# Kernel tuning notes

Hardware: AMD Instinct MI355X
Metric: run time of the kernel (lower is better)

Reference implementation:

```python
import jax, jax.numpy as jnp
import numpy as np

B, N, D, H, L, FF, CLS = 32, 196, 768, 12, 12, 3072, 1000
HD = D // H
EPS = 1e-5


def setup_inputs() -> dict:
    key = jax.random.key(0)
    ks = jax.random.split(key, 8)
    s = 0.02
    return dict(
        x=jax.random.normal(ks[0], (B, N, D), jnp.float32),
        pos_emb=jax.random.normal(ks[1], (1, N, D), jnp.float32) * 0.2,
        qkv_w=jax.random.normal(ks[2], (L, D, 3 * D), jnp.float32) * s,
        qkv_b=jnp.zeros((L, 3 * D), jnp.float32),
        proj_w=jax.random.normal(ks[3], (L, D, D), jnp.float32) * s,
        proj_b=jnp.zeros((L, D), jnp.float32),
        lin1_w=jax.random.normal(ks[4], (L, D, FF), jnp.float32) * s,
        lin1_b=jnp.zeros((L, FF), jnp.float32),
        lin2_w=jax.random.normal(ks[5], (L, FF, D), jnp.float32) * s,
        lin2_b=jnp.zeros((L, D), jnp.float32),
        pre_ln_w=jnp.ones((L, D), jnp.float32),
        pre_ln_b=jnp.zeros((L, D), jnp.float32),
        norm1_w=jnp.ones((L, D), jnp.float32),
        norm1_b=jnp.zeros((L, D), jnp.float32),
        attn_ln_w=jnp.ones((L, H, N, N), jnp.float32),
        attn_ln_b=jnp.zeros((L, H, N, N), jnp.float32),
        final_ln_w=jnp.ones((D,), jnp.float32),
        final_ln_b=jnp.zeros((D,), jnp.float32),
        pool_w=jax.random.normal(ks[6], (D, 1), jnp.float32) * s,
        pool_b=jnp.zeros((1,), jnp.float32),
        fc_w=jax.random.normal(ks[7], (D, CLS), jnp.float32) * s,
        fc_b=jnp.zeros((CLS,), jnp.float32),
    )


def _ln(x, w, b):
    mu = x.mean(-1, keepdims=True)
    var = ((x - mu) ** 2).mean(-1, keepdims=True)
    return (x - mu) * jax.lax.rsqrt(var + EPS) * w + b


def _forward(x, pos_emb, qkv_w, qkv_b, proj_w, proj_b, lin1_w, lin1_b,
             lin2_w, lin2_b, pre_ln_w, pre_ln_b, norm1_w, norm1_b,
             attn_ln_w, attn_ln_b, final_ln_w, final_ln_b,
             pool_w, pool_b, fc_w, fc_b):
    h = x + pos_emb  # (B,N,D)
    params = dict(qw=qkv_w, qb=qkv_b, pw=proj_w, pb=proj_b,
                  l1w=lin1_w, l1b=lin1_b, l2w=lin2_w, l2b=lin2_b,
                  prew=pre_ln_w, preb=pre_ln_b, n1w=norm1_w, n1b=norm1_b,
                  aw=attn_ln_w, ab=attn_ln_b)

    def step(carry, p):
        src, _ = carry
        y = _ln(src, p['prew'], p['preb'])
        qkv = (y @ p['qw'] + p['qb']).reshape(B, N, 3, H, HD)
        qkv = qkv.transpose(2, 0, 3, 1, 4)  # (3,B,H,N,HD)
        q, k, v = qkv[0], qkv[1], qkv[2]
        # grassmanian_point: project each head vector onto the unit sphere
        q = q / jnp.linalg.norm(q, axis=-1, keepdims=True)
        k = k / jnp.linalg.norm(k, axis=-1, keepdims=True)
        # ||q_i outer k_j||^2 over head_dim == sum_d q_id^2 * k_jd^2
        attn = jnp.einsum('bhid,bhjd->bhij', q * q, k * k)  # (B,H,N,N)
        # LayerNorm over (H,N,N) per batch element
        mu = attn.mean(axis=(1, 2, 3), keepdims=True)
        var = ((attn - mu) ** 2).mean(axis=(1, 2, 3), keepdims=True)
        attn = (attn - mu) * jax.lax.rsqrt(var + EPS) * p['aw'] + p['ab']
        out = jnp.einsum('bhij,bhjd->bhid', attn, v)
        out = out.transpose(0, 2, 1, 3).reshape(B, N, D)
        out = out @ p['pw'] + p['pb']
        src = _ln(src + out, p['n1w'], p['n1b'])
        ff = jax.nn.gelu(src @ p['l1w'] + p['l1b'], approximate=False)
        ff = ff @ p['l2w'] + p['l2b']
        return (src + ff, attn), None

    init = (h, jnp.zeros((B, H, N, N), x.dtype))
    (src, attn), _ = jax.lax.scan(step, init, params)
    xf = _ln(src, final_ln_w, final_ln_b)
    a = jax.nn.softmax(xf @ pool_w + pool_b, axis=1)  # (B,N,1) sequence pooling
    pooled = jnp.einsum('bnk,bnd->bd', a, xf)
    logits = pooled @ fc_w + fc_b
    return logits, attn


def reference(x, pos_emb, qkv_w, qkv_b, proj_w, proj_b, lin1_w, lin1_b,
              lin2_w, lin2_b, pre_ln_w, pre_ln_b, norm1_w, norm1_b,
              attn_ln_w, attn_ln_b, final_ln_w, final_ln_b,
              pool_w, pool_b, fc_w, fc_b):
    return _forward(x, pos_emb, qkv_w, qkv_b, proj_w, proj_b, lin1_w, lin1_b,
                    lin2_w, lin2_b, pre_ln_w, pre_ln_b, norm1_w, norm1_b,
                    attn_ln_w, attn_ln_b, final_ln_w, final_ln_b,
                    pool_w, pool_b, fc_w, fc_b)
```

## Files before the change

kernel.cpp:

```cpp
#include <hip/hip_runtime.h>
#include <hip/hip_bf16.h>

typedef unsigned short u16;
typedef __bf16 bf16x8 __attribute__((ext_vector_type(8)));
typedef _Float16 f16x8 __attribute__((ext_vector_type(8)));
typedef float f32x4 __attribute__((ext_vector_type(4)));
typedef u16 u16x8 __attribute__((ext_vector_type(8)));
typedef u16 u16x4 __attribute__((ext_vector_type(4)));

#define B_ 32
#define N_ 196
#define D_ 768
#define H_ 12
#define L_ 12
#define FF_ 3072
#define CLS_ 1000
#define HD_ 64
#define BH_ 384
#define NTOK_ 6272
#define NP_ 224
#define ATTN_PER_B_ 460992
#define NN_ 38416

__device__ inline u16 f2bf(float f){
    __bf16 h = (__bf16)f;
    return __builtin_bit_cast(u16, h);
}
__device__ inline float bf2f(u16 u){
    __bf16 h = __builtin_bit_cast(__bf16, u);
    return (float)h;
}
__device__ inline void split3(float v, u16& s0, u16& s1, u16& s2){
    s0 = f2bf(v);
    float r = v - bf2f(s0);
    s1 = f2bf(r);
    r = r - bf2f(s1);
    s2 = f2bf(r);
}
__device__ inline u16 f2h(float f){
    _Float16 h = (_Float16)f;
    return __builtin_bit_cast(u16, h);
}
__device__ inline float h2f(u16 u){
    _Float16 h = __builtin_bit_cast(_Float16, u);
    return (float)h;
}
__device__ inline void split2h(float v, u16& h0, u16& h1){
    h0 = f2h(v);
    h1 = f2h(v - h2f(h0));
}


__global__ __launch_bounds__(256)
void addpos_kernel(const float* __restrict__ x, const float* __restrict__ pos,
                   float* __restrict__ src){
    size_t gid = (size_t)blockIdx.x * 256 + threadIdx.x;
    size_t e = gid * 4;
    size_t tok = e / D_;
    size_t d = e % D_;
    size_t pe = (tok % N_) * D_ + d;
    float4 a = *(const float4*)(x + e);
    float4 p = *(const float4*)(pos + pe);
    float4 o = make_float4(a.x + p.x, a.y + p.y, a.z + p.z, a.w + p.w);
    *(float4*)(src + e) = o;
}

__global__ __launch_bounds__(256)
void wtrans_kernel(const float* __restrict__ in, u16* __restrict__ o0,
                   u16* __restrict__ o1, int K, int Nn){
    __shared__ float t[32][33];
    int n0 = blockIdx.x * 32, k0 = blockIdx.y * 32;
    int tx = threadIdx.x & 31, ty = threadIdx.x >> 5;
#pragma unroll
    for (int r = 0; r < 4; ++r)
        t[ty + 8*r][tx] = in[(size_t)(k0 + ty + 8*r) * Nn + n0 + tx];
    __syncthreads();
#pragma unroll
    for (int r = 0; r < 4; ++r){
        float v = t[tx][ty + 8*r];
        size_t oi = (size_t)(n0 + ty + 8*r) * K + k0 + tx;
        u16 a, b;
        split2h(v, a, b);
        o0[oi] = a; o1[oi] = b;
    }
}


__global__ __launch_bounds__(256)
void ln_row(const float* __restrict__ in, const float* __restrict__ w,
            const float* __restrict__ bb, float* __restrict__ outF,
            u16* __restrict__ o0, u16* __restrict__ o1){
    int row = blockIdx.x, tid = threadIdx.x;
    const float* base = in + (size_t)row * D_;
    float x0 = base[tid], x1 = base[tid + 256], x2 = base[tid + 512];
    float s = x0 + x1 + x2;
    float q = x0*x0 + x1*x1 + x2*x2;
    __shared__ float red[8];
    for (int o = 32; o > 0; o >>= 1){ s += __shfl_down(s, o); q += __shfl_down(q, o); }
    if ((tid & 63) == 0){ red[tid >> 6] = s; red[4 + (tid >> 6)] = q; }
    __syncthreads();
    s = red[0] + red[1] + red[2] + red[3];
    q = red[4] + red[5] + red[6] + red[7];
    float mu = s * (1.f / D_);
    float rv = rsqrtf(q * (1.f / D_) - mu * mu + 1e-5f);
#pragma unroll
    for (int t = 0; t < 3; ++t){
        int c = tid + t * 256;
        float x = (t == 0 ? x0 : (t == 1 ? x1 : x2));
        float val = (x - mu) * rv * w[c] + bb[c];
        size_t oi = (size_t)row * D_ + c;
        if (outF) outF[oi] = val;
        if (o0){
            u16 a, b;
            split2h(val, a, b);
            o0[oi] = a; o1[oi] = b;
        }
    }
}


template<int EPI>
__global__ __launch_bounds__(256)
void gemm_f16s2(const u16* __restrict__ A0, const u16* __restrict__ A1,
                const u16* __restrict__ B0, const u16* __restrict__ B1,
                const float* __restrict__ bias, const float* __restrict__ res,
                float* __restrict__ outF, u16* __restrict__ oH,
                u16* __restrict__ oL, int M, int Nn, int K){
    __shared__ u16 Lds[2][4][128 * 32];
    const int tid = threadIdx.x;
    const int w = tid >> 6, l = tid & 63;
    const int wr = w >> 1, wc = w & 1;
    const int nwg = gridDim.x;
    const int nbx = Nn >> 7;
    const int orig = blockIdx.x;
    const int qq = nwg >> 3, rr = nwg & 7;
    const int xcd = orig & 7, local = orig >> 3;
    const int wg = (xcd < rr ? xcd * (qq + 1) : rr * (qq + 1) + (xcd - rr) * qq) + local;
    const int m0 = (wg / nbx) * 128, n0 = (wg % nbx) * 128;
    const u16* gsrc = (w == 0 ? A0 : w == 1 ? A1 : w == 2 ? B0 : B1);
    const int rowbase = (w < 2 ? m0 : n0);
    const int lq = (l & 3) ^ ((l >> 3) & 3);
    const u16* gp = gsrc + (size_t)(rowbase + (l >> 2)) * K + lq * 8;
    const size_t gstep = (size_t)16 * K;
    f32x4 acc[4][4] = {};
    const int arow = l & 15;
    const int qsel = l >> 4;
    const int nsteps = K >> 5;

    auto stage = [&](int buf, int k0){
        u16* lbuf = &Lds[buf][w][0];
        const u16* gpk = gp + k0;
#pragma unroll
        for (int i = 0; i < 8; ++i){
            __builtin_amdgcn_global_load_lds(
                (const __attribute__((address_space(1))) unsigned int*)gpk,
                (__attribute__((address_space(3))) unsigned int*)(lbuf + i * 512),
                16, 0, 0);
            gpk += gstep;
        }
    };

    stage(0, 0);
    for (int step = 0; step < nsteps; ++step){
        const int cur = step & 1;
        __syncthreads();
        if (step + 1 < nsteps) stage(1 - cur, (step + 1) << 5);
        f16x8 a0[4], a1[4], b0[4], b1[4];
#pragma unroll
        for (int m = 0; m < 4; ++m){
            int row = wr * 64 + m * 16 + arow;
            int off = row * 32 + ((qsel ^ ((row >> 1) & 3)) * 8);
            a0[m] = __builtin_bit_cast(f16x8, *(const u16x8*)&Lds[cur][0][off]);
            a1[m] = __builtin_bit_cast(f16x8, *(const u16x8*)&Lds[cur][1][off]);
        }
#pragma unroll
        for (int n = 0; n < 4; ++n){
            int row = wc * 64 + n * 16 + arow;
            int off = row * 32 + ((qsel ^ ((row >> 1) & 3)) * 8);
            b0[n] = __builtin_bit_cast(f16x8, *(const u16x8*)&Lds[cur][2][off]);
            b1[n] = __builtin_bit_cast(f16x8, *(const u16x8*)&Lds[cur][3][off]);
        }
#pragma unroll
        for (int m = 0; m < 4; ++m)
#pragma unroll
            for (int n = 0; n < 4; ++n){
                acc[m][n] = __builtin_amdgcn_mfma_f32_16x16x32_f16(a1[m], b0[n], acc[m][n], 0, 0, 0);
                acc[m][n] = __builtin_amdgcn_mfma_f32_16x16x32_f16(a0[m], b1[n], acc[m][n], 0, 0, 0);
                acc[m][n] = __builtin_amdgcn_mfma_f32_16x16x32_f16(a0[m], b0[n], acc[m][n], 0, 0, 0);
            }
    }
    const int r4 = (l >> 4) * 4, c16 = l & 15;
#pragma unroll
    for (int m = 0; m < 4; ++m){
#pragma unroll
        for (int n = 0; n < 4; ++n){
            int colg = n0 + wc*64 + n*16 + c16;
            float bv = bias[colg];
#pragma unroll
            for (int r = 0; r < 4; ++r){
                int rowg = m0 + wr*64 + m*16 + r4 + r;
                size_t oi = (size_t)rowg * Nn + colg;
                float v = acc[m][n][r] + bv;
                if (EPI == 0){
                    outF[oi] = v;
                } else if (EPI == 1){
                    v = 0.5f * v * (1.0f + erff(v * 0.70710678118654752f));
                    u16 a, b;
                    split2h(v, a, b);
                    oH[oi] = a; oL[oi] = b;
                } else {
                    outF[oi] = v + res[oi];
                }
            }
        }
    }
}


__global__ __launch_bounds__(256)
void qkprep_kernel(const float* __restrict__ QKV,
                   u16* __restrict__ Q0, u16* __restrict__ Q1, u16* __restrict__ Q2,
                   u16* __restrict__ K0, u16* __restrict__ K1, u16* __restrict__ K2,
                   u16* __restrict__ VT0, u16* __restrict__ VT1){
    __shared__ float vbuf[NP_][65];
    int bh = blockIdx.x;
    int b = bh / H_, h = bh % H_;
    int w = threadIdx.x >> 6, l = threadIdx.x & 63;
    size_t base = (size_t)bh * (NP_ * HD_);
    for (int n = w; n < NP_; n += 4){
        size_t oi = base + (size_t)n * HD_ + l;
        if (n < N_){
            const float* row = QKV + (size_t)(b * N_ + n) * (3 * D_) + h * HD_;
            float qv = row[l], kv = row[D_ + l], vv = row[2 * D_ + l];
            double qs = (double)qv * (double)qv, ks = (double)kv * (double)kv;
            double qr = qs, kr = ks;
            for (int o = 32; o > 0; o >>= 1){ qr += __shfl_xor(qr, o); kr += __shfl_xor(kr, o); }
            float q2 = (float)(qs / qr), k2 = (float)(ks / kr);
            u16 a, bb, c;
            split3(q2, a, bb, c);
            Q0[oi] = a; Q1[oi] = bb; Q2[oi] = c;
            split3(k2, a, bb, c);
            K0[oi] = a; K1[oi] = bb; K2[oi] = c;
            vbuf[n][l] = vv;
        } else {
            Q0[oi] = 0; Q1[oi] = 0; Q2[oi] = 0;
            K0[oi] = 0; K1[oi] = 0; K2[oi] = 0;
            vbuf[n][l] = 0.f;
        }
    }
    __syncthreads();
    size_t vtb = (size_t)bh * (HD_ * NP_);
    for (int idx = threadIdx.x; idx < HD_ * NP_; idx += 256){
        int d = idx / NP_, n = idx % NP_;
        u16 a, bb;
        split2h(vbuf[n][d], a, bb);
        VT0[vtb + idx] = a; VT1[vtb + idx] = bb;
    }
}


#define SPAD 72

__global__ __launch_bounds__(256)
void score_mfma3(const u16* __restrict__ Q0, const u16* __restrict__ Q1,
                 const u16* __restrict__ Q2,
                 const u16* __restrict__ K0, const u16* __restrict__ K1,
                 const u16* __restrict__ K2,
                 float* __restrict__ S, double2* __restrict__ part){
    __shared__ u16 Ql[3][32][SPAD];
    __shared__ u16 Kl[3][32][SPAD];
    __shared__ double red2[8];
    int i0 = blockIdx.x * 32;
    int bh = blockIdx.y;
    int tid = threadIdx.x;
    size_t base = (size_t)bh * (NP_ * HD_);
    {
        int r = tid >> 3, q = tid & 7;
        size_t src = base + (size_t)(i0 + r) * HD_ + q * 8;
        *(u16x8*)&Ql[0][r][q * 8] = *(const u16x8*)(Q0 + src);
        *(u16x8*)&Ql[1][r][q * 8] = *(const u16x8*)(Q1 + src);
        *(u16x8*)&Ql[2][r][q * 8] = *(const u16x8*)(Q2 + src);
    }
    const int w = tid >> 6, l = tid & 63;
    const int wm = w >> 1, wn = w & 1;
    const int arow = l & 15, kg0 = (l >> 4) * 8;
    const int r4 = (l >> 4) * 4, c16 = l & 15;
    double dsum = 0.0, dsq = 0.0;
    for (int jt = 0; jt < 7; ++jt){
        __syncthreads();
        {
            int r = tid >> 3, q = tid & 7;
            size_t src = base + (size_t)(jt * 32 + r) * HD_ + q * 8;
            *(u16x8*)&Kl[0][r][q * 8] = *(const u16x8*)(K0 + src);
            *(u16x8*)&Kl[1][r][q * 8] = *(const u16x8*)(K1 + src);
            *(u16x8*)&Kl[2][r][q * 8] = *(const u16x8*)(K2 + src);
        }
        __syncthreads();
        f32x4 acc = {};
#pragma unroll
        for (int kk = 0; kk < 2; ++kk){
            int kg = kk * 32 + kg0;
            bf16x8 a0 = __builtin_bit_cast(bf16x8, *(const u16x8*)&Ql[0][wm*16 + arow][kg]);
            bf16x8 a1 = __builtin_bit_cast(bf16x8, *(const u16x8*)&Ql[1][wm*16 + arow][kg]);
            bf16x8 a2 = __builtin_bit_cast(bf16x8, *(const u16x8*)&Ql[2][wm*16 + arow][kg]);
            bf16x8 b0 = __builtin_bit_cast(bf16x8, *(const u16x8*)&Kl[0][wn*16 + arow][kg]);
            bf16x8 b1 = __builtin_bit_cast(bf16x8, *(const u16x8*)&Kl[1][wn*16 + arow][kg]);
            bf16x8 b2 = __builtin_bit_cast(bf16x8, *(const u16x8*)&Kl[2][wn*16 + arow][kg]);
            acc = __builtin_amdgcn_mfma_f32_16x16x32_bf16(a2, b0, acc, 0, 0, 0);
            acc = __builtin_amdgcn_mfma_f32_16x16x32_bf16(a1, b1, acc, 0, 0, 0);
            acc = __builtin_amdgcn_mfma_f32_16x16x32_bf16(a0, b2, acc, 0, 0, 0);
            acc = __builtin_amdgcn_mfma_f32_16x16x32_bf16(a1, b0, acc, 0, 0, 0);
            acc = __builtin_amdgcn_mfma_f32_16x16x32_bf16(a0, b1, acc, 0, 0, 0);
            acc = __builtin_amdgcn_mfma_f32_16x16x32_bf16(a0, b0, acc, 0, 0, 0);
        }
#pragma unroll
        for (int r = 0; r < 4; ++r){
            int i = i0 + wm * 16 + r4 + r;
            int j = jt * 32 + wn * 16 + c16;
            if (i < N_ && j < N_){
                float v = acc[r];
                S[((size_t)bh * N_ + i) * N_ + j] = v;
                dsum += (double)v;
                dsq += (double)v * (double)v;
            }
        }
    }
    for (int o = 32; o > 0; o >>= 1){
        dsum += __shfl_down(dsum, o);
        dsq  += __shfl_down(dsq, o);
    }
    __syncthreads();
    if ((tid & 63) == 0){ red2[tid >> 6] = dsum; red2[4 + (tid >> 6)] = dsq; }
    __syncthreads();
    if (tid == 0){
        int b = bh / H_, h = bh % H_;
        part[(size_t)b * 84 + h * 7 + blockIdx.x] =
            make_double2(red2[0] + red2[1] + red2[2] + red2[3],
                         red2[4] + red2[5] + red2[6] + red2[7]);
    }
}

__global__ __launch_bounds__(64)
void reduceMS_kernel(const double2* __restrict__ part, float2* __restrict__ musig){
    int b = blockIdx.x, tid = threadIdx.x;
    double s = 0.0, q = 0.0;
    for (int i = tid; i < 84; i += 64){
        double2 p = part[(size_t)b * 84 + i];
        s += p.x; q += p.y;
    }
    for (int o = 32; o > 0; o >>= 1){ s += __shfl_down(s, o); q += __shfl_down(q, o); }
    if (tid == 0){
        double mu = s / (double)ATTN_PER_B_;
        double var = q / (double)ATTN_PER_B_ - mu * mu;
        musig[b] = make_float2((float)mu, (float)(1.0 / sqrt(var + 1e-5)));
    }
}


__global__ __launch_bounds__(256)
void attnnorm_f16(float* __restrict__ S, const float* __restrict__ wv,
                  const float* __restrict__ bv, const float2* __restrict__ musig,
                  u16* __restrict__ AS0, u16* __restrict__ AS1, int writeS){
    int gid = blockIdx.x * 256 + threadIdx.x;
    int jg = gid % 56;
    int rem = gid / 56;
    int i = rem % NP_;
    int bh = rem / NP_;
    int b = bh / H_, h = bh % H_;
    float2 ms = musig[b];
    u16x4 p0, p1;
#pragma unroll
    for (int t = 0; t < 4; ++t){
        int j = jg * 4 + t;
        float val = 0.f;
        if (i < N_ && j < N_){
            size_t si = ((size_t)bh * N_ + i) * N_ + j;
            size_t wi = ((size_t)h * N_ + i) * N_ + j;
            float s = S[si];
            val = (s - ms.x) * ms.y * wv[wi] + bv[wi];
            if (writeS) S[si] = val;
        }
        u16 a, bb;
        split2h(val, a, bb);
        p0[t] = a; p1[t] = bb;
    }
    size_t oo = (size_t)bh * (NP_ * NP_) + (size_t)i * NP_ + jg * 4;
    *(u16x4*)&AS0[oo] = p0;
    *(u16x4*)&AS1[oo] = p1;
}


__global__ __launch_bounds__(256)
void pv_f16s2(const u16* __restrict__ AS0, const u16* __restrict__ AS1,
              const u16* __restrict__ VT0, const u16* __restrict__ VT1,
              u16* __restrict__ PA0, u16* __restrict__ PA1){
    __shared__ u16 Al[2][32][40];
    __shared__ u16 Vl[2][64][40];
    int i0 = blockIdx.x * 32;
    int bh = blockIdx.y;
    int b = bh / H_, h = bh % H_;
    int tid = threadIdx.x;
    size_t abase = (size_t)bh * (NP_ * NP_) + (size_t)i0 * NP_;
    size_t vbase = (size_t)bh * (HD_ * NP_);
    const int w = tid >> 6, l = tid & 63;
    const int arow = l & 15, kg0 = (l >> 4) * 8;
    const int r4 = (l >> 4) * 4, c16 = l & 15;
    f32x4 acc[2] = {};
    for (int k0 = 0; k0 < NP_; k0 += 32){
        __syncthreads();
        {
            int s = tid >> 7, rem = tid & 127;
            int r = rem >> 2, q = rem & 3;
            const u16* src = (s == 0 ? AS0 : AS1);
            *(u16x8*)&Al[s][r][q * 8] = *(const u16x8*)(src + abase + (size_t)r * NP_ + k0 + q * 8);
        }
#pragma unroll
        for (int it = 0; it < 2; ++it){
            int c = tid + it * 256;
            int s = c >> 8, rem = c & 255;
            int r = rem >> 2, q = rem & 3;
            const u16* src = (s == 0 ? VT0 : VT1);
            *(u16x8*)&Vl[s][r][q * 8] = *(const u16x8*)(src + vbase + (size_t)r * NP_ + k0 + q * 8);
        }
        __syncthreads();
        f16x8 a0[2], a1[2];
#pragma unroll
        for (int m = 0; m < 2; ++m){
            a0[m] = __builtin_bit_cast(f16x8, *(const u16x8*)&Al[0][m*16 + arow][kg0]);
            a1[m] = __builtin_bit_cast(f16x8, *(const u16x8*)&Al[1][m*16 + arow][kg0]);
        }
        f16x8 b0 = __builtin_bit_cast(f16x8, *(const u16x8*)&Vl[0][w*16 + arow][kg0]);
        f16x8 b1 = __builtin_bit_cast(f16x8, *(const u16x8*)&Vl[1][w*16 + arow][kg0]);
#pragma unroll
        for (int m = 0; m < 2; ++m){
            acc[m] = __builtin_amdgcn_mfma_f32_16x16x32_f16(a1[m], b1, acc[m], 0, 0, 0);
            acc[m] = __builtin_amdgcn_mfma_f32_16x16x32_f16(a1[m], b0, acc[m], 0, 0, 0);
            acc[m] = __builtin_amdgcn_mfma_f32_16x16x32_f16(a0[m], b1, acc[m], 0, 0, 0);
            acc[m] = __builtin_amdgcn_mfma_f32_16x16x32_f16(a0[m], b0, acc[m], 0, 0, 0);
        }
    }
#pragma unroll
    for (int m = 0; m < 2; ++m)
#pragma unroll
        for (int r = 0; r < 4; ++r){
            int i = i0 + m * 16 + r4 + r;
            if (i < N_){
                size_t oi = ((size_t)b * N_ + i) * D_ + h * HD_ + w * 16 + c16;
                u16 s0, s1;
                split2h(acc[m][r], s0, s1);
                PA0[oi] = s0; PA1[oi] = s1;
            }
        }
}


__global__ __launch_bounds__(256)
void rowdot_kernel(const float* __restrict__ xf, const float* __restrict__ pw,
                   const float* __restrict__ pb, float* __restrict__ sraw){
    int row = blockIdx.x, tid = threadIdx.x;
    const float* base = xf + (size_t)row * D_;
    float s = base[tid] * pw[tid] + base[tid + 256] * pw[tid + 256] + base[tid + 512] * pw[tid + 512];
    __shared__ float red[4];
    for (int o = 32; o > 0; o >>= 1) s += __shfl_xor(s, o);
    if ((tid & 63) == 0) red[tid >> 6] = s;
    __syncthreads();
    if (tid == 0) sraw[row] = red[0] + red[1] + red[2] + red[3] + pb[0];
}

__global__ __launch_bounds__(256)
void softmax196_kernel(const float* __restrict__ sraw, float* __restrict__ aw){
    int b = blockIdx.x, tid = threadIdx.x;
    __shared__ float red[8];
    float v = (tid < N_) ? sraw[b * N_ + tid] : -3.0e38f;
    float m = v;
    for (int o = 32; o > 0; o >>= 1) m = fmaxf(m, __shfl_xor(m, o));
    if ((tid & 63) == 0) red[tid >> 6] = m;
    __syncthreads();
    float M = fmaxf(fmaxf(red[0], red[1]), fmaxf(red[2], red[3]));
    float e = (tid < N_) ? expf(v - M) : 0.f;
    float s = e;
    for (int o = 32; o > 0; o >>= 1) s += __shfl_xor(s, o);
    if ((tid & 63) == 0) red[4 + (tid >> 6)] = s;
    __syncthreads();
    float S = red[4] + red[5] + red[6] + red[7];
    if (tid < N_) aw[b * N_ + tid] = e / S;
}

__global__ __launch_bounds__(256)
void poolmat_kernel(const float* __restrict__ aw, const float* __restrict__ xf,
                    float* __restrict__ pooled){
    int b = blockIdx.y;
    int d = blockIdx.x * 256 + threadIdx.x;
    float acc = 0.f;
    for (int n = 0; n < N_; ++n)
        acc += aw[b * N_ + n] * xf[((size_t)b * N_ + n) * D_ + d];
    pooled[b * D_ + d] = acc;
}

__global__ __launch_bounds__(256)
void fc_kernel(const float* __restrict__ pooled, const float* __restrict__ fw,
               const float* __restrict__ fb, float* __restrict__ out){
    int b = blockIdx.y;
    int c = blockIdx.x * 256 + threadIdx.x;
    if (c >= CLS_) return;
    float acc = fb[c];
    for (int d = 0; d < D_; ++d)
        acc += pooled[b * D_ + d] * fw[(size_t)d * CLS_ + c];
    out[b * CLS_ + c] = acc;
}

__global__ __launch_bounds__(256)
void zero_logits(float* __restrict__ out){
    out[blockIdx.x * 256 + threadIdx.x] = 0.f;
}


extern "C" void kernel_launch(void* const* d_in, const int* in_sizes, int n_in,
                              void* d_out, int out_size, void* d_ws, size_t ws_size,
                              hipStream_t stream){
    const float* x        = (const float*)d_in[0];
    const float* pos_emb  = (const float*)d_in[1];
    const float* qkv_w    = (const float*)d_in[2];
    const float* qkv_b    = (const float*)d_in[3];
    const float* proj_w   = (const float*)d_in[4];
    const float* proj_b   = (const float*)d_in[5];
    const float* lin1_w   = (const float*)d_in[6];
    const float* lin1_b   = (const float*)d_in[7];
    const float* lin2_w   = (const float*)d_in[8];
    const float* lin2_b   = (const float*)d_in[9];
    const float* pre_ln_w = (const float*)d_in[10];
    const float* pre_ln_b = (const float*)d_in[11];
    const float* norm1_w  = (const float*)d_in[12];
    const float* norm1_b  = (const float*)d_in[13];
    const float* attn_ln_w= (const float*)d_in[14];
    const float* attn_ln_b= (const float*)d_in[15];
    const float* fln_w    = (const float*)d_in[16];
    const float* fln_b    = (const float*)d_in[17];
    const float* pool_w   = (const float*)d_in[18];
    const float* pool_b   = (const float*)d_in[19];
    const float* fc_w     = (const float*)d_in[20];
    const float* fc_b     = (const float*)d_in[21];

    float* dout = (float*)d_out;
    float* S = dout + (size_t)B_ * CLS_;

    char* ws = (char*)d_ws;
    size_t off = 0;
    auto alloc = [&](size_t bytes)->char*{
        char* p = ws + off;
        off += (bytes + 255) & ~(size_t)255;
        return p;
    };
    float* SRC   = (float*)alloc((size_t)NTOK_ * D_ * 4);
    float* Yb    = (float*)alloc((size_t)NTOK_ * D_ * 4);
    float* TMP   = (float*)alloc((size_t)NTOK_ * D_ * 4);
    float* QKV   = (float*)alloc((size_t)NTOK_ * 3 * D_ * 4);
    u16*   A0    = (u16*)  alloc((size_t)NTOK_ * D_ * 2);
    u16*   A1    = (u16*)  alloc((size_t)NTOK_ * D_ * 2);
    u16*   W0    = (u16*)  alloc((size_t)FF_ * D_ * 2);
    u16*   W1    = (u16*)  alloc((size_t)FF_ * D_ * 2);
    u16*   F0    = (u16*)  alloc((size_t)NTOK_ * FF_ * 2);
    u16*   F1    = (u16*)  alloc((size_t)NTOK_ * FF_ * 2);
    u16*   Q0b   = (u16*)  alloc((size_t)BH_ * NP_ * HD_ * 2);
    u16*   Q1b   = (u16*)  alloc((size_t)BH_ * NP_ * HD_ * 2);
    u16*   Q2b   = (u16*)  alloc((size_t)BH_ * NP_ * HD_ * 2);
    u16*   K0b   = (u16*)  alloc((size_t)BH_ * NP_ * HD_ * 2);
    u16*   K1b   = (u16*)  alloc((size_t)BH_ * NP_ * HD_ * 2);
    u16*   K2b   = (u16*)  alloc((size_t)BH_ * NP_ * HD_ * 2);
    u16*   VT0   = (u16*)  alloc((size_t)BH_ * HD_ * NP_ * 2);
    u16*   VT1   = (u16*)  alloc((size_t)BH_ * HD_ * NP_ * 2);
    double2* PART= (double2*)alloc((size_t)B_ * 84 * 16);
    float2* MUSIG= (float2*)alloc((size_t)B_ * 8);
    float* SRAW  = (float*)alloc((size_t)NTOK_ * 4);
    float* AW    = (float*)alloc((size_t)NTOK_ * 4);
    float* POOLED= (float*)alloc((size_t)B_ * D_ * 4);
    u16* AS0 = F0, *AS1 = F1;

    if (ws_size < off){
        zero_logits<<<(B_ * CLS_) / 256, 256, 0, stream>>>(dout);
        return;
    }

    const int cvt_blocks = NTOK_ * D_ / (256 * 4);
    const int an_blocks = (int)((size_t)BH_ * NP_ * NP_ / (256 * 4));

    addpos_kernel<<<cvt_blocks, 256, 0, stream>>>(x, pos_emb, SRC);

    for (int l = 0; l < L_; ++l){
        const float* qw  = qkv_w  + (size_t)l * D_ * 3 * D_;
        const float* qb  = qkv_b  + (size_t)l * 3 * D_;
        const float* pw  = proj_w + (size_t)l * D_ * D_;
        const float* pb  = proj_b + (size_t)l * D_;
        const float* l1w = lin1_w + (size_t)l * D_ * FF_;
        const float* l1b = lin1_b + (size_t)l * FF_;
        const float* l2w = lin2_w + (size_t)l * FF_ * D_;
        const float* l2b = lin2_b + (size_t)l * D_;
        const float* prw = pre_ln_w + (size_t)l * D_;
        const float* prb = pre_ln_b + (size_t)l * D_;
        const float* n1w = norm1_w + (size_t)l * D_;
        const float* n1b = norm1_b + (size_t)l * D_;
        const float* awl = attn_ln_w + (size_t)l * H_ * N_ * N_;
        const float* abl = attn_ln_b + (size_t)l * H_ * N_ * N_;

        ln_row<<<NTOK_, 256, 0, stream>>>(SRC, prw, prb, nullptr, A0, A1);
        wtrans_kernel<<<dim3(3 * D_ / 32, D_ / 32), 256, 0, stream>>>(qw, W0, W1, D_, 3 * D_);
        gemm_f16s2<0><<<(3 * D_ / 128) * (NTOK_ / 128), 256, 0, stream>>>(
            A0, A1, W0, W1, qb, nullptr, QKV, nullptr, nullptr, NTOK_, 3 * D_, D_);
        qkprep_kernel<<<BH_, 256, 0, stream>>>(QKV, Q0b, Q1b, Q2b, K0b, K1b, K2b,
                                               VT0, VT1);
        score_mfma3<<<dim3(7, BH_), 256, 0, stream>>>(Q0b, Q1b, Q2b, K0b, K1b, K2b,
                                                      S, PART);
        reduceMS_kernel<<<B_, 64, 0, stream>>>(PART, MUSIG);
        attnnorm_f16<<<an_blocks, 256, 0, stream>>>(S, awl, abl, MUSIG, AS0, AS1,
                                                    l == L_ - 1 ? 1 : 0);
        pv_f16s2<<<dim3(7, BH_), 256, 0, stream>>>(AS0, AS1, VT0, VT1, A0, A1);
        wtrans_kernel<<<dim3(D_ / 32, D_ / 32), 256, 0, stream>>>(pw, W0, W1, D_, D_);
        gemm_f16s2<2><<<(D_ / 128) * (NTOK_ / 128), 256, 0, stream>>>(
            A0, A1, W0, W1, pb, SRC, TMP, nullptr, nullptr, NTOK_, D_, D_);
        ln_row<<<NTOK_, 256, 0, stream>>>(TMP, n1w, n1b, SRC, A0, A1);
        wtrans_kernel<<<dim3(FF_ / 32, D_ / 32), 256, 0, stream>>>(l1w, W0, W1, D_, FF_);
        gemm_f16s2<1><<<(FF_ / 128) * (NTOK_ / 128), 256, 0, stream>>>(
            A0, A1, W0, W1, l1b, nullptr, nullptr, F0, F1, NTOK_, FF_, D_);
        wtrans_kernel<<<dim3(D_ / 32, FF_ / 32), 256, 0, stream>>>(l2w, W0, W1, FF_, D_);
        gemm_f16s2<2><<<(D_ / 128) * (NTOK_ / 128), 256, 0, stream>>>(
            F0, F1, W0, W1, l2b, SRC, SRC, nullptr, nullptr, NTOK_, D_, FF_);
    }

    ln_row<<<NTOK_, 256, 0, stream>>>(SRC, fln_w, fln_b, Yb, nullptr, nullptr);
    rowdot_kernel<<<NTOK_, 256, 0, stream>>>(Yb, pool_w, pool_b, SRAW);
    softmax196_kernel<<<B_, 256, 0, stream>>>(SRAW, AW);
    poolmat_kernel<<<dim3(D_ / 256, B_), 256, 0, stream>>>(AW, Yb, POOLED);
    fc_kernel<<<dim3((CLS_ + 255) / 256, B_), 256, 0, stream>>>(POOLED, fc_w, fc_b, dout);
}
```

Measured before the change: 7.306 ms.

## Fuse attention normalization into PV kernel and use f16x2 split for scores

```diff
diff --git a/kernel.cpp b/kernel.cpp
--- a/kernel.cpp
+++ b/kernel.cpp
@@ -2,7 +2,6 @@
 #include <hip/hip_bf16.h>
 
 typedef unsigned short u16;
-typedef __bf16 bf16x8 __attribute__((ext_vector_type(8)));
 typedef _Float16 f16x8 __attribute__((ext_vector_type(8)));
 typedef float f32x4 __attribute__((ext_vector_type(4)));
 typedef u16 u16x8 __attribute__((ext_vector_type(8)));
@@ -22,21 +21,6 @@
 #define ATTN_PER_B_ 460992
 #define NN_ 38416
 
-__device__ inline u16 f2bf(float f){
-    __bf16 h = (__bf16)f;
-    return __builtin_bit_cast(u16, h);
-}
-__device__ inline float bf2f(u16 u){
-    __bf16 h = __builtin_bit_cast(__bf16, u);
-    return (float)h;
-}
-__device__ inline void split3(float v, u16& s0, u16& s1, u16& s2){
-    s0 = f2bf(v);
-    float r = v - bf2f(s0);
-    s1 = f2bf(r);
-    r = r - bf2f(s1);
-    s2 = f2bf(r);
-}
 __device__ inline u16 f2h(float f){
     _Float16 h = (_Float16)f;
     return __builtin_bit_cast(u16, h);
@@ -219,8 +203,8 @@
 
 __global__ __launch_bounds__(256)
 void qkprep_kernel(const float* __restrict__ QKV,
-                   u16* __restrict__ Q0, u16* __restrict__ Q1, u16* __restrict__ Q2,
-                   u16* __restrict__ K0, u16* __restrict__ K1, u16* __restrict__ K2,
+                   u16* __restrict__ Q0, u16* __restrict__ Q1,
+                   u16* __restrict__ K0, u16* __restrict__ K1,
                    u16* __restrict__ VT0, u16* __restrict__ VT1){
     __shared__ float vbuf[NP_][65];
     int bh = blockIdx.x;
@@ -236,15 +220,15 @@
             double qr = qs, kr = ks;
             for (int o = 32; o > 0; o >>= 1){ qr += __shfl_xor(qr, o); kr += __shfl_xor(kr, o); }
             float q2 = (float)(qs / qr), k2 = (float)(ks / kr);
-            u16 a, bb, c;
-            split3(q2, a, bb, c);
-            Q0[oi] = a; Q1[oi] = bb; Q2[oi] = c;
-            split3(k2, a, bb, c);
-            K0[oi] = a; K1[oi] = bb; K2[oi] = c;
+            u16 a, bb;
+            split2h(q2, a, bb);
+            Q0[oi] = a; Q1[oi] = bb;
+            split2h(k2, a, bb);
+            K0[oi] = a; K1[oi] = bb;
             vbuf[n][l] = vv;
         } else {
-            Q0[oi] = 0; Q1[oi] = 0; Q2[oi] = 0;
-            K0[oi] = 0; K1[oi] = 0; K2[oi] = 0;
+            Q0[oi] = 0; Q1[oi] = 0;
+            K0[oi] = 0; K1[oi] = 0;
             vbuf[n][l] = 0.f;
         }
     }
@@ -262,13 +246,11 @@
 #define SPAD 72
 
 __global__ __launch_bounds__(256)
-void score_mfma3(const u16* __restrict__ Q0, const u16* __restrict__ Q1,
-                 const u16* __restrict__ Q2,
+void score_f16s2(const u16* __restrict__ Q0, const u16* __restrict__ Q1,
                  const u16* __restrict__ K0, const u16* __restrict__ K1,
-                 const u16* __restrict__ K2,
                  float* __restrict__ S, double2* __restrict__ part){
-    __shared__ u16 Ql[3][32][SPAD];
-    __shared__ u16 Kl[3][32][SPAD];
+    __shared__ u16 Ql[2][32][SPAD];
+    __shared__ u16 Kl[2][32][SPAD];
     __shared__ double red2[8];
     int i0 = blockIdx.x * 32;
     int bh = blockIdx.y;
@@ -279,7 +261,6 @@
         size_t src = base + (size_t)(i0 + r) * HD_ + q * 8;
         *(u16x8*)&Ql[0][r][q * 8] = *(const u16x8*)(Q0 + src);
         *(u16x8*)&Ql[1][r][q * 8] = *(const u16x8*)(Q1 + src);
-        *(u16x8*)&Ql[2][r][q * 8] = *(const u16x8*)(Q2 + src);
     }
     const int w = tid >> 6, l = tid & 63;
     const int wm = w >> 1, wn = w & 1;
@@ -293,25 +274,20 @@
             size_t src = base + (size_t)(jt * 32 + r) * HD_ + q * 8;
             *(u16x8*)&Kl[0][r][q * 8] = *(const u16x8*)(K0 + src);
             *(u16x8*)&Kl[1][r][q * 8] = *(const u16x8*)(K1 + src);
-            *(u16x8*)&Kl[2][r][q * 8] = *(const u16x8*)(K2 + src);
         }
         __syncthreads();
         f32x4 acc = {};
 #pragma unroll
         for (int kk = 0; kk < 2; ++kk){
             int kg = kk * 32 + kg0;
-            bf16x8 a0 = __builtin_bit_cast(bf16x8, *(const u16x8*)&Ql[0][wm*16 + arow][kg]);
-            bf16x8 a1 = __builtin_bit_cast(bf16x8, *(const u16x8*)&Ql[1][wm*16 + arow][kg]);
-            bf16x8 a2 = __builtin_bit_cast(bf16x8, *(const u16x8*)&Ql[2][wm*16 + arow][kg]);
-            bf16x8 b0 = __builtin_bit_cast(bf16x8, *(const u16x8*)&Kl[0][wn*16 + arow][kg]);
-            bf16x8 b1 = __builtin_bit_cast(bf16x8, *(const u16x8*)&Kl[1][wn*16 + arow][kg]);
-            bf16x8 b2 = __builtin_bit_cast(bf16x8, *(const u16x8*)&Kl[2][wn*16 + arow][kg]);
-            acc = __builtin_amdgcn_mfma_f32_16x16x32_bf16(a2, b0, acc, 0, 0, 0);
-            acc = __builtin_amdgcn_mfma_f32_16x16x32_bf16(a1, b1, acc, 0, 0, 0);
-            acc = __builtin_amdgcn_mfma_f32_16x16x32_bf16(a0, b2, acc, 0, 0, 0);
-            acc = __builtin_amdgcn_mfma_f32_16x16x32_bf16(a1, b0, acc, 0, 0, 0);
-            acc = __builtin_amdgcn_mfma_f32_16x16x32_bf16(a0, b1, acc, 0, 0, 0);
-            acc = __builtin_amdgcn_mfma_f32_16x16x32_bf16(a0, b0, acc, 0, 0, 0);
+            f16x8 a0 = __builtin_bit_cast(f16x8, *(const u16x8*)&Ql[0][wm*16 + arow][kg]);
+            f16x8 a1 = __builtin_bit_cast(f16x8, *(const u16x8*)&Ql[1][wm*16 + arow][kg]);
+            f16x8 b0 = __builtin_bit_cast(f16x8, *(const u16x8*)&Kl[0][wn*16 + arow][kg]);
+            f16x8 b1 = __builtin_bit_cast(f16x8, *(const u16x8*)&Kl[1][wn*16 + arow][kg]);
+            acc = __builtin_amdgcn_mfma_f32_16x16x32_f16(a1, b1, acc, 0, 0, 0);
+            acc = __builtin_amdgcn_mfma_f32_16x16x32_f16(a1, b0, acc, 0, 0, 0);
+            acc = __builtin_amdgcn_mfma_f32_16x16x32_f16(a0, b1, acc, 0, 0, 0);
+            acc = __builtin_amdgcn_mfma_f32_16x16x32_f16(a0, b0, acc, 0, 0, 0);
         }
 #pragma unroll
         for (int r = 0; r < 4; ++r){
@@ -358,61 +334,67 @@
 
 
 __global__ __launch_bounds__(256)
-void attnnorm_f16(float* __restrict__ S, const float* __restrict__ wv,
-                  const float* __restrict__ bv, const float2* __restrict__ musig,
-                  u16* __restrict__ AS0, u16* __restrict__ AS1, int writeS){
-    int gid = blockIdx.x * 256 + threadIdx.x;
-    int jg = gid % 56;
-    int rem = gid / 56;
-    int i = rem % NP_;
-    int bh = rem / NP_;
-    int b = bh / H_, h = bh % H_;
+void attnnorm_final(float* __restrict__ S, const float* __restrict__ wv,
+                    const float* __restrict__ bv, const float2* __restrict__ musig){
+    size_t idx = ((size_t)blockIdx.x * 256 + threadIdx.x) * 4;
+    int b = (int)(idx / ATTN_PER_B_);
+    int wi = (int)(idx % ATTN_PER_B_);
     float2 ms = musig[b];
-    u16x4 p0, p1;
-#pragma unroll
-    for (int t = 0; t < 4; ++t){
-        int j = jg * 4 + t;
-        float val = 0.f;
-        if (i < N_ && j < N_){
-            size_t si = ((size_t)bh * N_ + i) * N_ + j;
-            size_t wi = ((size_t)h * N_ + i) * N_ + j;
-            float s = S[si];
-            val = (s - ms.x) * ms.y * wv[wi] + bv[wi];
-            if (writeS) S[si] = val;
-        }
-        u16 a, bb;
-        split2h(val, a, bb);
-        p0[t] = a; p1[t] = bb;
-    }
-    size_t oo = (size_t)bh * (NP_ * NP_) + (size_t)i * NP_ + jg * 4;
-    *(u16x4*)&AS0[oo] = p0;
-    *(u16x4*)&AS1[oo] = p1;
-}
-
-
-__global__ __launch_bounds__(256)
-void pv_f16s2(const u16* __restrict__ AS0, const u16* __restrict__ AS1,
-              const u16* __restrict__ VT0, const u16* __restrict__ VT1,
-              u16* __restrict__ PA0, u16* __restrict__ PA1){
+    float4 s = *(const float4*)(S + idx);
+    float4 w = *(const float4*)(wv + wi);
+    float4 bb = *(const float4*)(bv + wi);
+    s.x = (s.x - ms.x) * ms.y * w.x + bb.x;
+    s.y = (s.y - ms.x) * ms.y * w.y + bb.y;
+    s.z = (s.z - ms.x) * ms.y * w.z + bb.z;
+    s.w = (s.w - ms.x) * ms.y * w.w + bb.w;
+    *(float4*)(S + idx) = s;
+}
+
+
+__global__ __launch_bounds__(256)
+void pv_norm(const float* __restrict__ S, const float* __restrict__ wv,
+             const float* __restrict__ bv, const float2* __restrict__ musig,
+             const u16* __restrict__ VT0, const u16* __restrict__ VT1,
+             u16* __restrict__ PA0, u16* __restrict__ PA1){
     __shared__ u16 Al[2][32][40];
     __shared__ u16 Vl[2][64][40];
     int i0 = blockIdx.x * 32;
     int bh = blockIdx.y;
     int b = bh / H_, h = bh % H_;
     int tid = threadIdx.x;
-    size_t abase = (size_t)bh * (NP_ * NP_) + (size_t)i0 * NP_;
+    float2 ms = musig[b];
     size_t vbase = (size_t)bh * (HD_ * NP_);
     const int w = tid >> 6, l = tid & 63;
     const int arow = l & 15, kg0 = (l >> 4) * 8;
     const int r4 = (l >> 4) * 4, c16 = l & 15;
+    const int sr = tid >> 3, sc4 = (tid & 7) * 4;
     f32x4 acc[2] = {};
     for (int k0 = 0; k0 < NP_; k0 += 32){
         __syncthreads();
         {
-            int s = tid >> 7, rem = tid & 127;
-            int r = rem >> 2, q = rem & 3;
-            const u16* src = (s == 0 ? AS0 : AS1);
-            *(u16x8*)&Al[s][r][q * 8] = *(const u16x8*)(src + abase + (size_t)r * NP_ + k0 + q * 8);
+            int i = i0 + sr, j = k0 + sc4;
+            u16x4 p0, p1;
+            if (i < N_ && j + 3 < N_){
+                size_t si = ((size_t)bh * N_ + i) * N_ + j;
+                size_t wi = ((size_t)h * N_ + i) * N_ + j;
+                float4 sv = *(const float4*)(S + si);
+                float4 wvv = *(const float4*)(wv + wi);
+                float4 bvv = *(const float4*)(bv + wi);
+                float v0 = (sv.x - ms.x) * ms.y * wvv.x + bvv.x;
+                float v1 = (sv.y - ms.x) * ms.y * wvv.y + bvv.y;
+                float v2 = (sv.z - ms.x) * ms.y * wvv.z + bvv.z;
+                float v3 = (sv.w - ms.x) * ms.y * wvv.w + bvv.w;
+                u16 t0, t1;
+                split2h(v0, t0, t1); p0[0] = t0; p1[0] = t1;
+                split2h(v1, t0, t1); p0[1] = t0; p1[1] = t1;
+                split2h(v2, t0, t1); p0[2] = t0; p1[2] = t1;
+                split2h(v3, t0, t1); p0[3] = t0; p1[3] = t1;
+            } else {
+                p0[0]=p0[1]=p0[2]=p0[3]=0;
+                p1[0]=p1[1]=p1[2]=p1[3]=0;
+            }
+            *(u16x4*)&Al[0][sr][sc4] = p0;
+            *(u16x4*)&Al[1][sr][sc4] = p1;
         }
 #pragma unroll
         for (int it = 0; it < 2; ++it){
@@ -563,10 +545,8 @@
     u16*   F1    = (u16*)  alloc((size_t)NTOK_ * FF_ * 2);
     u16*   Q0b   = (u16*)  alloc((size_t)BH_ * NP_ * HD_ * 2);
     u16*   Q1b   = (u16*)  alloc((size_t)BH_ * NP_ * HD_ * 2);
-    u16*   Q2b   = (u16*)  alloc((size_t)BH_ * NP_ * HD_ * 2);
     u16*   K0b   = (u16*)  alloc((size_t)BH_ * NP_ * HD_ * 2);
     u16*   K1b   = (u16*)  alloc((size_t)BH_ * NP_ * HD_ * 2);
-    u16*   K2b   = (u16*)  alloc((size_t)BH_ * NP_ * HD_ * 2);
     u16*   VT0   = (u16*)  alloc((size_t)BH_ * HD_ * NP_ * 2);
     u16*   VT1   = (u16*)  alloc((size_t)BH_ * HD_ * NP_ * 2);
     double2* PART= (double2*)alloc((size_t)B_ * 84 * 16);
@@ -574,7 +554,6 @@
     float* SRAW  = (float*)alloc((size_t)NTOK_ * 4);
     float* AW    = (float*)alloc((size_t)NTOK_ * 4);
     float* POOLED= (float*)alloc((size_t)B_ * D_ * 4);
-    u16* AS0 = F0, *AS1 = F1;
 
     if (ws_size < off){
         zero_logits<<<(B_ * CLS_) / 256, 256, 0, stream>>>(dout);
@@ -582,7 +561,7 @@
     }
 
     const int cvt_blocks = NTOK_ * D_ / (256 * 4);
-    const int an_blocks = (int)((size_t)BH_ * NP_ * NP_ / (256 * 4));
+    const int anf_blocks = (int)((size_t)B_ * ATTN_PER_B_ / (256 * 4));
 
     addpos_kernel<<<cvt_blocks, 256, 0, stream>>>(x, pos_emb, SRC);
 
@@ -606,14 +585,12 @@
         wtrans_kernel<<<dim3(3 * D_ / 32, D_ / 32), 256, 0, stream>>>(qw, W0, W1, D_, 3 * D_);
         gemm_f16s2<0><<<(3 * D_ / 128) * (NTOK_ / 128), 256, 0, stream>>>(
             A0, A1, W0, W1, qb, nullptr, QKV, nullptr, nullptr, NTOK_, 3 * D_, D_);
-        qkprep_kernel<<<BH_, 256, 0, stream>>>(QKV, Q0b, Q1b, Q2b, K0b, K1b, K2b,
-                                               VT0, VT1);
-        score_mfma3<<<dim3(7, BH_), 256, 0, stream>>>(Q0b, Q1b, Q2b, K0b, K1b, K2b,
-                                                      S, PART);
+        qkprep_kernel<<<BH_, 256, 0, stream>>>(QKV, Q0b, Q1b, K0b, K1b, VT0, VT1);
+        score_f16s2<<<dim3(7, BH_), 256, 0, stream>>>(Q0b, Q1b, K0b, K1b, S, PART);
         reduceMS_kernel<<<B_, 64, 0, stream>>>(PART, MUSIG);
-        attnnorm_f16<<<an_blocks, 256, 0, stream>>>(S, awl, abl, MUSIG, AS0, AS1,
-                                                    l == L_ - 1 ? 1 : 0);
-        pv_f16s2<<<dim3(7, BH_), 256, 0, stream>>>(AS0, AS1, VT0, VT1, A0, A1);
+        pv_norm<<<dim3(7, BH_), 256, 0, stream>>>(S, awl, abl, MUSIG, VT0, VT1, A0, A1);
+        if (l == L_ - 1)
+            attnnorm_final<<<anf_blocks, 256, 0, stream>>>(S, awl, abl, MUSIG);
         wtrans_kernel<<<dim3(D_ / 32, D_ / 32), 256, 0, stream>>>(pw, W0, W1, D_, D_);
         gemm_f16s2<2><<<(D_ / 128) * (NTOK_ / 128), 256, 0, stream>>>(
             A0, A1, W0, W1, pb, SRC, TMP, nullptr, nullptr, NTOK_, D_, D_);
```

After: 6.764 ms, median of 3. 7.4% less time.
